# Kernel optimization log

Measured on AMD Instinct MI355X. Metric: run time of the kernel, lower is better.

The kernel has to match this reference:

```python
import jax, jax.numpy as jnp
import numpy as np

D, H, DH, DFF, K = 512, 8, 64, 2048, 31
B, T = 8, 1024


def _ln(x, g, b):
    m = x.mean(-1, keepdims=True)
    v = ((x - m) ** 2).mean(-1, keepdims=True)
    return (x - m) / jnp.sqrt(v + 1e-5) * g + b


def _silu(x):
    return x * jax.nn.sigmoid(x)


def _pe(t, d):
    i = jnp.arange(t, dtype=jnp.float32)[:, None]
    j = jnp.arange(0, d, 2, dtype=jnp.float32)
    ang = i * (1.0 / (10000.0 ** (j / d)))
    pe = jnp.zeros((t, d), jnp.float32)
    pe = pe.at[:, 0::2].set(jnp.sin(ang))
    pe = pe.at[:, 1::2].set(jnp.cos(ang))
    return pe


def setup_inputs() -> dict:
    key = jax.random.key(0)
    ks = iter(jax.random.split(key, 40))
    s = 0.02
    d = {
        'x': jax.random.normal(next(ks), (B, T, D), jnp.float32),
        # FF module 1
        'ff1_ln_g': jnp.ones((D,), jnp.float32), 'ff1_ln_b': jnp.zeros((D,), jnp.float32),
        'ff1_w1': jax.random.normal(next(ks), (D, DFF), jnp.float32) * s,
        'ff1_b1': jnp.zeros((DFF,), jnp.float32),
        'ff1_w2': jax.random.normal(next(ks), (DFF, D), jnp.float32) * s,
        'ff1_b2': jnp.zeros((D,), jnp.float32),
        # MHSA
        'mha_ln_g': jnp.ones((D,), jnp.float32), 'mha_ln_b': jnp.zeros((D,), jnp.float32),
        'wq': jax.random.normal(next(ks), (H, D, DH), jnp.float32) * s,
        'bq': jnp.zeros((H, DH), jnp.float32),
        'wk': jax.random.normal(next(ks), (H, D, DH), jnp.float32) * s,
        'bk': jnp.zeros((H, DH), jnp.float32),
        'wv': jax.random.normal(next(ks), (H, D, DH), jnp.float32) * s,
        'bv': jnp.zeros((H, DH), jnp.float32),
        'wo': jax.random.normal(next(ks), (D, D), jnp.float32) * s,
        'bo': jnp.zeros((D,), jnp.float32),
        # Conv module
        'cv_ln_g': jnp.ones((D,), jnp.float32), 'cv_ln_b': jnp.zeros((D,), jnp.float32),
        'cv_w1': jax.random.normal(next(ks), (2 * D, D), jnp.float32) * s,
        'cv_b1': jnp.zeros((2 * D,), jnp.float32),
        'cv_wd': jax.random.normal(next(ks), (D, D, K), jnp.float32) * s,
        'cv_bn_g': jnp.ones((D,), jnp.float32), 'cv_bn_b': jnp.zeros((D,), jnp.float32),
        'cv_w2': jax.random.normal(next(ks), (D, D), jnp.float32) * s,
        'cv_b2': jnp.zeros((D,), jnp.float32),
        # FF module 2
        'ff2_ln_g': jnp.ones((D,), jnp.float32), 'ff2_ln_b': jnp.zeros((D,), jnp.float32),
        'ff2_w1': jax.random.normal(next(ks), (D, DFF), jnp.float32) * s,
        'ff2_b1': jnp.zeros((DFF,), jnp.float32),
        'ff2_w2': jax.random.normal(next(ks), (DFF, D), jnp.float32) * s,
        'ff2_b2': jnp.zeros((D,), jnp.float32),
        # final layer norm
        'fin_g': jnp.ones((D,), jnp.float32), 'fin_b': jnp.zeros((D,), jnp.float32),
    }
    return d


def _block(x, p):
    def ffn(x, g, b, w1, b1, w2, b2):
        y = _silu(_ln(x, g, b) @ w1 + b1) @ w2 + b2
        return x + y  # FeedForwardModule internal residual

    # x = x + 0.5 * ff_1(x)
    x = x + 0.5 * ffn(x, p['ff1_ln_g'], p['ff1_ln_b'], p['ff1_w1'], p['ff1_b1'], p['ff1_w2'], p['ff1_b2'])

    # MHSA module (with its own internal residual), then block residual
    y = _ln(x, p['mha_ln_g'], p['mha_ln_b']) + _pe(x.shape[1], x.shape[2])
    q = jnp.einsum('btd,hde->bhte', y, p['wq']) + p['bq'][None, :, None, :]
    k = jnp.einsum('btd,hde->bhte', y, p['wk']) + p['bk'][None, :, None, :]
    v = jnp.einsum('btd,hde->bhte', y, p['wv']) + p['bv'][None, :, None, :]
    scores = jnp.einsum('bhtd,bhsd->bhts', q, k) * (1.0 / np.sqrt(DH))
    attn = jax.nn.softmax(scores, axis=-1)
    o = jnp.einsum('bhts,bhsd->bhtd', attn, v)
    # faithful to original: raw view [B,H,T,dh] -> [B,T,H*dh] (no transpose)
    o = o.reshape(x.shape[0], x.shape[1], H * DH)
    o = o @ p['wo'] + p['bo']
    x = x + (x + o)

    # Convolution module (internal residual), then block residual
    y = _ln(x, p['cv_ln_g'], p['cv_ln_b']).swapaxes(1, 2)  # [B,D,T]
    y = jnp.einsum('ed,bdt->bet', p['cv_w1'], y) + p['cv_b1'][None, :, None]
    a, g = jnp.split(y, 2, axis=1)
    y = a * jax.nn.sigmoid(g)  # GLU over channel dim
    y = jax.lax.conv_general_dilated(y, p['cv_wd'], (1,), [(K // 2, K // 2)],
                                     dimension_numbers=('NCH', 'OIH', 'NCH'))
    # BatchNorm1d in training mode: batch stats over (batch, time), biased variance
    m = y.mean((0, 2), keepdims=True)
    var = ((y - m) ** 2).mean((0, 2), keepdims=True)
    y = (y - m) / jnp.sqrt(var + 1e-5) * p['cv_bn_g'][None, :, None] + p['cv_bn_b'][None, :, None]
    y = _silu(y)
    y = jnp.einsum('ed,bdt->bet', p['cv_w2'], y) + p['cv_b2'][None, :, None]
    y = y.swapaxes(1, 2)
    x = x + (x + y)

    # x = x + 0.5 * ff_2(x)
    x = x + 0.5 * ffn(x, p['ff2_ln_g'], p['ff2_ln_b'], p['ff2_w1'], p['ff2_b1'], p['ff2_w2'], p['ff2_b2'])

    return _ln(x, p['fin_g'], p['fin_b'])


def reference(x, ff1_ln_g, ff1_ln_b, ff1_w1, ff1_b1, ff1_w2, ff1_b2,
              mha_ln_g, mha_ln_b, wq, bq, wk, bk, wv, bv, wo, bo,
              cv_ln_g, cv_ln_b, cv_w1, cv_b1, cv_wd, cv_bn_g, cv_bn_b, cv_w2, cv_b2,
              ff2_ln_g, ff2_ln_b, ff2_w1, ff2_b1, ff2_w2, ff2_b2,
              fin_g, fin_b):
    p = dict(ff1_ln_g=ff1_ln_g, ff1_ln_b=ff1_ln_b, ff1_w1=ff1_w1, ff1_b1=ff1_b1,
             ff1_w2=ff1_w2, ff1_b2=ff1_b2, mha_ln_g=mha_ln_g, mha_ln_b=mha_ln_b,
             wq=wq, bq=bq, wk=wk, bk=bk, wv=wv, bv=bv, wo=wo, bo=bo,
             cv_ln_g=cv_ln_g, cv_ln_b=cv_ln_b, cv_w1=cv_w1, cv_b1=cv_b1, cv_wd=cv_wd,
             cv_bn_g=cv_bn_g, cv_bn_b=cv_bn_b, cv_w2=cv_w2, cv_b2=cv_b2,
             ff2_ln_g=ff2_ln_g, ff2_ln_b=ff2_ln_b, ff2_w1=ff2_w1, ff2_b1=ff2_b1,
             ff2_w2=ff2_w2, ff2_b2=ff2_b2, fin_g=fin_g, fin_b=fin_b)
    return _block(x, p)
```

## Files before the change

### kernel.cpp

```cpp
#include <hip/hip_runtime.h>


typedef __attribute__((ext_vector_type(4))) float f32x4;
typedef __attribute__((ext_vector_type(8))) short short8;
typedef __attribute__((ext_vector_type(4))) short s16x4;

__device__ __forceinline__ float bfs2f(short s) {
  unsigned u = ((unsigned)(unsigned short)s) << 16;
  float f; __builtin_memcpy(&f, &u, 4); return f;
}
__device__ __forceinline__ short f2bfs(float f) {
  unsigned u; __builtin_memcpy(&u, &f, 4);
  u = (u + 0x7FFFu + ((u >> 16) & 1u)) >> 16;
  return (short)u;
}
__device__ __forceinline__ float sigmoidf_(float x) { return 1.f / (1.f + __expf(-x)); }

#define GLOADLDS(gsrc, ldst) \
  __builtin_amdgcn_global_load_lds((__attribute__((address_space(1))) void*)(gsrc), \
                                   (__attribute__((address_space(3))) void*)(ldst), 16, 0, 0)

#define VMCNT_ASM(n) asm volatile("s_waitcnt vmcnt(" #n ")" ::: "memory")
template<int N> __device__ __forceinline__ void vmcnt_wait() {
  if      constexpr (N == 0)  VMCNT_ASM(0);
  else if constexpr (N == 2)  VMCNT_ASM(2);
  else if constexpr (N == 3)  VMCNT_ASM(3);
  else if constexpr (N == 4)  VMCNT_ASM(4);
  else if constexpr (N == 6)  VMCNT_ASM(6);
  else if constexpr (N == 8)  VMCNT_ASM(8);
  else                        VMCNT_ASM(0);
}
#define MEMFENCE asm volatile("" ::: "memory")

enum { EPI_SILU = 0, EPI_BBIAS = 1, EPI_RES = 2, EPI_QKV = 3, EPI_F32 = 6 };

template<int BM, int BN, int WM, int WN, int EPI>
__global__ __launch_bounds__(256) void gemm_bt(
    const short* __restrict__ A, int lda, long zAh, long zAl,
    const short* __restrict__ BT, int ldbt, long zBh, long zBl,
    int K, int Kdec,
    void* C, int ldc, long zCh, long zCl, int zdiv,
    const float* bias, const float* bias2, const float* bias3,
    const float* resid, float alpha, float beta)
{
  constexpr int FM = BM / (WM * 16), FN = BN / (WN * 16);
  constexpr int AIT = (BM * 4) / 256, BIT = (BN * 4) / 256;
  constexpr int L = AIT + BIT;
  __shared__ short sA[3][BM * 32];
  __shared__ short sB[3][BN * 32];
  const int tid = threadIdx.x;
  const int zmask = (1 << zdiv) - 1;
  const int zhi = (int)(blockIdx.z >> zdiv);
  const int zlo = (int)(blockIdx.z & zmask);
  A  += (long)zhi * zAh + (long)zlo * zAl;
  BT += (long)zhi * zBh + (long)zlo * zBl;
  char* cbase = (char*)C + (long)zhi * zCh + (long)zlo * zCl;
  const int m0 = blockIdx.x * BM, n0 = blockIdx.y * BN;
  const int Keff = K - (zlo == zmask ? Kdec : 0);

  auto stage = [&](int buf, int k0) {
#pragma unroll
    for (int it = 0; it < AIT; ++it) {
      int idx = it * 256 + tid;
      GLOADLDS(A + (long)(m0 + (idx >> 2)) * lda + k0 + (idx & 3) * 8, &sA[buf][idx * 8]);
    }
#pragma unroll
    for (int it = 0; it < BIT; ++it) {
      int idx = it * 256 + tid;
      GLOADLDS(BT + (long)(n0 + (idx >> 2)) * ldbt + k0 + (idx & 3) * 8, &sB[buf][idx * 8]);
    }
  };

  f32x4 acc[FM][FN];
#pragma unroll
  for (int i = 0; i < FM; ++i) {
#pragma unroll
    for (int j = 0; j < FN; ++j) acc[i][j] = (f32x4){0.f, 0.f, 0.f, 0.f};
  }
  const int lane = tid & 63, wid = tid >> 6;
  const int wm = wid / WN, wn = wid % WN;
  const int lr = lane & 15, kg = lane >> 4;
  const int aRow = wm * (BM / WM), bRow = wn * (BN / WN);

  const int nt = Keff >> 5;
  stage(0, 0);
  stage(1, 32);
  vmcnt_wait<L>();
  __builtin_amdgcn_s_barrier();

  int cur = 0, sbuf = 2;
  for (int t = 0; t < nt; ++t) {
    const bool st = (t + 2 < nt);
    if (st) stage(sbuf, (t + 2) * 32);
    short8 af[FM], bfr[FN];
#pragma unroll
    for (int mi = 0; mi < FM; ++mi)
      af[mi] = *(const short8*)&sA[cur][(aRow + mi * 16 + lr) * 32 + kg * 8];
#pragma unroll
    for (int ni = 0; ni < FN; ++ni)
      bfr[ni] = *(const short8*)&sB[cur][(bRow + ni * 16 + lr) * 32 + kg * 8];
    __builtin_amdgcn_s_setprio(1);
#pragma unroll
    for (int mi = 0; mi < FM; ++mi) {
#pragma unroll
      for (int ni = 0; ni < FN; ++ni)
        acc[mi][ni] = __builtin_amdgcn_mfma_f32_16x16x32_bf16(af[mi], bfr[ni], acc[mi][ni], 0, 0, 0);
    }
    __builtin_amdgcn_s_setprio(0);
    if (st) vmcnt_wait<L>(); else vmcnt_wait<0>();
    __builtin_amdgcn_s_barrier();
    cur = (cur == 2) ? 0 : cur + 1;
    sbuf = (sbuf == 2) ? 0 : sbuf + 1;
  }

  const int baseRow = m0 + aRow, baseCol = n0 + bRow;
#pragma unroll
  for (int mi = 0; mi < FM; ++mi) {
#pragma unroll
    for (int ni = 0; ni < FN; ++ni) {
      const int col = baseCol + ni * 16 + lr;
#pragma unroll
      for (int r = 0; r < 4; ++r) {
        const int row = baseRow + mi * 16 + kg * 4 + r;
        float v = acc[mi][ni][r];
        if (EPI == EPI_SILU) {
          v += bias[col];
          v = v * sigmoidf_(v);
          ((short*)cbase)[(long)row * ldc + col] = f2bfs(v);
        } else if (EPI == EPI_BBIAS) {
          v += bias[col];
          ((short*)cbase)[(long)row * ldc + col] = f2bfs(v);
        } else if (EPI == EPI_RES) {
          v += bias[col];
          float rv = resid[(long)row * ldc + col];
          ((float*)cbase)[(long)row * ldc + col] = alpha * rv + beta * v;
        } else if (EPI == EPI_QKV) {
          if (col < 512)       v = (v + bias[col]) * 0.125f;
          else if (col < 1024) v += bias2[col - 512];
          else                 v += bias3[col - 1024];
          ((short*)cbase)[(long)row * ldc + col] = f2bfs(v);
        } else if (EPI == EPI_F32) {
          ((float*)cbase)[(long)row * ldc + col] = v;
        }
      }
    }
  }
}

__global__ __launch_bounds__(256) void conv_tap(
    const short* __restrict__ glu,
    const short* __restrict__ wdP,
    short* __restrict__ parts)
{
  __shared__ short sA[2][144 * 32];
  const int tid = threadIdx.x;
  const int bid = blockIdx.x;
  const int cc = bid & 7, j = bid >> 3;
  const int y = cc >> 1, kg = cc & 1;
  const int x = j & 7, b = j >> 3;
  const int m0 = x * 128, n0 = y * 128;
  const short* Arow0 = glu + ((long)b * 1056 + m0 + 1 + kg * 16) * 512;
  short* cbase = parts + (long)kg * (8192L * 512) + (long)b * (1024L * 512);

  const int lane = tid & 63, wid = tid >> 6;
  const int wm = wid >> 1, wn = wid & 1;
  const int lr = lane & 15, kgr = lane >> 4;
  const int aRow = wm * 64, bRow = wn * 64;

  const short* Bp = wdP + (long)((n0 + bRow) >> 4) * (512L * 512)
                  + (long)(kg * 256) * 512 + lane * 8;
  const long NSTR = 512L * 512;

  auto stageA = [&](int buf, int ib) {
#pragma unroll
    for (int it = 0; it < 3; ++it) {
      int idx = it * 256 + tid;
      if (idx < 576) {
        GLOADLDS(Arow0 + (long)(idx >> 2) * 512 + ib * 32 + (idx & 3) * 8,
                 &sA[buf][idx * 8]);
      }
    }
  };

  f32x4 acc[4][4];
#pragma unroll
  for (int i = 0; i < 4; ++i) {
#pragma unroll
    for (int jj = 0; jj < 4; ++jj) acc[i][jj] = (f32x4){0.f, 0.f, 0.f, 0.f};
  }
  short8 b0[4], b1[4];

  stageA(0, 0);
  MEMFENCE;
#pragma unroll
  for (int ni = 0; ni < 4; ++ni)
    b0[ni] = *(const short8*)(Bp + ni * NSTR);
  MEMFENCE;
  vmcnt_wait<4>();
  __builtin_amdgcn_s_barrier();

  int cur = 0;
  for (int ib = 0; ib < 16; ++ib) {
    if (ib + 1 < 16) stageA(cur ^ 1, ib + 1);
    MEMFENCE;
#pragma unroll
    for (int kk = 0; kk < 16; ++kk) {
      const long noff = (kk + 1 < 16) ? (long)((kk + 1) * 16 + ib) * 512
                                      : (long)(ib + 1) * 512;
      if ((kk & 1) == 0) {
#pragma unroll
        for (int ni = 0; ni < 4; ++ni)
          b1[ni] = *(const short8*)(Bp + noff + ni * NSTR);
      } else {
#pragma unroll
        for (int ni = 0; ni < 4; ++ni)
          b0[ni] = *(const short8*)(Bp + noff + ni * NSTR);
      }
      short8 af[4];
#pragma unroll
      for (int mi = 0; mi < 4; ++mi)
        af[mi] = *(const short8*)&sA[cur][(kk + aRow + mi * 16 + lr) * 32 + kgr * 8];
      __builtin_amdgcn_s_setprio(1);
      if ((kk & 1) == 0) {
#pragma unroll
        for (int mi = 0; mi < 4; ++mi) {
#pragma unroll
          for (int ni = 0; ni < 4; ++ni)
            acc[mi][ni] = __builtin_amdgcn_mfma_f32_16x16x32_bf16(af[mi], b0[ni], acc[mi][ni], 0, 0, 0);
        }
      } else {
#pragma unroll
        for (int mi = 0; mi < 4; ++mi) {
#pragma unroll
          for (int ni = 0; ni < 4; ++ni)
            acc[mi][ni] = __builtin_amdgcn_mfma_f32_16x16x32_bf16(af[mi], b1[ni], acc[mi][ni], 0, 0, 0);
        }
      }
      __builtin_amdgcn_s_setprio(0);
    }
    vmcnt_wait<4>();
    __builtin_amdgcn_s_barrier();
    cur ^= 1;
  }
  vmcnt_wait<0>();

  const int baseRow = m0 + aRow, baseCol = n0 + bRow;
#pragma unroll
  for (int mi = 0; mi < 4; ++mi) {
#pragma unroll
    for (int ni = 0; ni < 4; ++ni) {
      const int col = baseCol + ni * 16 + lr;
#pragma unroll
      for (int r = 0; r < 4; ++r) {
        const int row = baseRow + mi * 16 + kgr * 4 + r;
        cbase[(long)row * 512 + col] = f2bfs(acc[mi][ni][r]);
      }
    }
  }
}

__global__ __launch_bounds__(256) void flash_attn(
    const short* __restrict__ qkv,
    const short* __restrict__ vt,
    short* __restrict__ out)
{
  __shared__ short sQ[64 * 64];
  __shared__ short sK[64 * 64];
  __shared__ short sV[64 * 64];
  __shared__ short sP[4][16 * 64];
  const int tid = threadIdx.x;
  const int lane = tid & 63, w = tid >> 6;
  const int lr = lane & 15, kg = lane >> 4;
  const int bh = (int)blockIdx.z;
  const int b = bh >> 3, h = bh & 7;
  const int q0 = blockIdx.x * 64;
  const short* qbase = qkv + (long)b * 1024 * 1536 + h * 64;
  const short* kbase = qbase + 512;
  const short* vtb = vt + (long)bh * 65536;

#pragma unroll
  for (int it = 0; it < 2; ++it) {
    int idx = it * 256 + tid;
    int row = idx >> 3, c = (idx & 7) ^ (row & 7);
    GLOADLDS(qbase + (long)(q0 + row) * 1536 + c * 8, &sQ[idx * 8]);
  }
  __syncthreads();
  short8 bq[2];
#pragma unroll
  for (int ks = 0; ks < 2; ++ks)
    bq[ks] = *(const short8*)&sQ[(w * 16 + lr) * 64 + ((ks * 4 + kg) ^ (lr & 7)) * 8];

  f32x4 po[4];
#pragma unroll
  for (int mi = 0; mi < 4; ++mi) po[mi] = (f32x4){0.f, 0.f, 0.f, 0.f};
  float m = -3.0e38f, l = 0.f;

  for (int s0 = 0; s0 < 1024; s0 += 64) {
#pragma unroll
    for (int it = 0; it < 2; ++it) {
      int idx = it * 256 + tid;
      int row = idx >> 3, c = (idx & 7) ^ (row & 7);
      GLOADLDS(kbase + (long)(s0 + row) * 1536 + c * 8, &sK[idx * 8]);
    }
#pragma unroll
    for (int it = 0; it < 2; ++it) {
      int idx = it * 256 + tid;
      int row = idx >> 3, c = (idx & 7) ^ (row & 7);
      GLOADLDS(vtb + (long)row * 1024 + s0 + c * 8, &sV[idx * 8]);
    }
    __syncthreads();

    f32x4 as[4];
#pragma unroll
    for (int mi = 0; mi < 4; ++mi) as[mi] = (f32x4){0.f, 0.f, 0.f, 0.f};
    __builtin_amdgcn_s_setprio(1);
#pragma unroll
    for (int ks = 0; ks < 2; ++ks) {
#pragma unroll
      for (int mi = 0; mi < 4; ++mi) {
        short8 ak = *(const short8*)&sK[(mi * 16 + lr) * 64 + ((ks * 4 + kg) ^ (lr & 7)) * 8];
        as[mi] = __builtin_amdgcn_mfma_f32_16x16x32_bf16(ak, bq[ks], as[mi], 0, 0, 0);
      }
    }
    __builtin_amdgcn_s_setprio(0);

    float rmax = as[0][0];
#pragma unroll
    for (int mi = 0; mi < 4; ++mi) {
#pragma unroll
      for (int r = 0; r < 4; ++r) rmax = fmaxf(rmax, as[mi][r]);
    }
    rmax = fmaxf(rmax, __shfl_xor(rmax, 16));
    rmax = fmaxf(rmax, __shfl_xor(rmax, 32));
    const float mn = fmaxf(m, rmax);
    const float sc = __expf(m - mn);
    float p[4][4];
    float rsum = 0.f;
#pragma unroll
    for (int mi = 0; mi < 4; ++mi) {
#pragma unroll
      for (int r = 0; r < 4; ++r) { p[mi][r] = __expf(as[mi][r] - mn); rsum += p[mi][r]; }
    }
    rsum += __shfl_xor(rsum, 16);
    rsum += __shfl_xor(rsum, 32);
    l = l * sc + rsum;
    m = mn;
#pragma unroll
    for (int mi = 0; mi < 4; ++mi) {
#pragma unroll
      for (int r = 0; r < 4; ++r) po[mi][r] *= sc;
    }
#pragma unroll
    for (int mi = 0; mi < 4; ++mi) {
      s16x4 pk;
#pragma unroll
      for (int r = 0; r < 4; ++r) pk[r] = f2bfs(p[mi][r]);
      *(s16x4*)&sP[w][lr * 64 + ((mi ^ (lr & 3)) * 16 + kg * 4)] = pk;
    }
    __builtin_amdgcn_s_setprio(1);
#pragma unroll
    for (int ks = 0; ks < 2; ++ks) {
      short8 bp = *(const short8*)&sP[w][lr * 64 + (((ks * 2 + (kg >> 1)) ^ (lr & 3)) * 16 + (kg & 1) * 8)];
#pragma unroll
      for (int mi = 0; mi < 4; ++mi) {
        short8 av = *(const short8*)&sV[(mi * 16 + lr) * 64 + ((ks * 4 + kg) ^ (lr & 7)) * 8];
        po[mi] = __builtin_amdgcn_mfma_f32_16x16x32_bf16(av, bp, po[mi], 0, 0, 0);
      }
    }
    __builtin_amdgcn_s_setprio(0);
    __syncthreads();
  }

  const float inv = 1.f / l;
  const int t2 = q0 + w * 16 + lr;
  const int n = h * 1024 + t2;
  short* ob = out + ((long)b * 1024 + (n >> 3)) * 512 + (n & 7) * 64;
#pragma unroll
  for (int mi = 0; mi < 4; ++mi) {
    s16x4 o;
#pragma unroll
    for (int r = 0; r < 4; ++r) o[r] = f2bfs(po[mi][r] * inv);
    *(s16x4*)&ob[mi * 16 + kg * 4] = o;
  }
}

__global__ __launch_bounds__(256) void reduce_bn(
    const short* __restrict__ parts, long pstride,
    short* __restrict__ z, float* stats)
{
  const int r0 = blockIdx.x * 16;
  const int c = threadIdx.x * 2;
  float s0 = 0.f, s1 = 0.f, q0 = 0.f, q1 = 0.f;
#pragma unroll 4
  for (int r = 0; r < 16; ++r) {
    const long idx = (long)(r0 + r) * 512 + c;
    int p0 = *(const int*)&parts[idx];
    int p1 = *(const int*)&parts[idx + pstride];
    float a0 = bfs2f((short)(p0 & 0xffff)) + bfs2f((short)(p1 & 0xffff));
    float a1 = bfs2f((short)(p0 >> 16)) + bfs2f((short)(p1 >> 16));
    int zo = ((int)(unsigned short)f2bfs(a0)) | (((int)(unsigned short)f2bfs(a1)) << 16);
    *(int*)&z[idx] = zo;
    s0 += a0; s1 += a1; q0 += a0 * a0; q1 += a1 * a1;
  }
  atomicAdd(&stats[c], s0);
  atomicAdd(&stats[c + 1], s1);
  atomicAdd(&stats[512 + c], q0);
  atomicAdd(&stats[512 + c + 1], q1);
}

template<int ADDPE, int OUTF32>
__global__ __launch_bounds__(256) void ln_rows(
    const float* __restrict__ X, const float* __restrict__ g, const float* __restrict__ b,
    const float* __restrict__ pe, void* __restrict__ Y)
{
  const int row = blockIdx.x * 4 + (threadIdx.x >> 6);
  const int lane = threadIdx.x & 63;
  const int c0 = lane * 8;
  const float* src = X + (long)row * 512 + c0;
  f32x4 a = *(const f32x4*)src, c = *(const f32x4*)(src + 4);
  float x[8] = {a[0], a[1], a[2], a[3], c[0], c[1], c[2], c[3]};
  float s = 0.f, q = 0.f;
#pragma unroll
  for (int j = 0; j < 8; ++j) { s += x[j]; q += x[j] * x[j]; }
#pragma unroll
  for (int off = 32; off > 0; off >>= 1) { s += __shfl_xor(s, off); q += __shfl_xor(q, off); }
  const float mean = s * (1.f / 512.f);
  const float var = q * (1.f / 512.f) - mean * mean;
  const float rstd = rsqrtf(var + 1e-5f);
  f32x4 g0 = *(const f32x4*)(g + c0), g1 = *(const f32x4*)(g + c0 + 4);
  f32x4 b0 = *(const f32x4*)(b + c0), b1 = *(const f32x4*)(b + c0 + 4);
  float gg[8] = {g0[0], g0[1], g0[2], g0[3], g1[0], g1[1], g1[2], g1[3]};
  float bb[8] = {b0[0], b0[1], b0[2], b0[3], b1[0], b1[1], b1[2], b1[3]};
  float y[8];
#pragma unroll
  for (int j = 0; j < 8; ++j) {
    y[j] = (x[j] - mean) * rstd * gg[j] + bb[j];
    if (ADDPE) y[j] += pe[(long)(row & 1023) * 512 + c0 + j];
  }
  if (OUTF32) {
    float* dst = (float*)Y + (long)row * 512 + c0;
    *(f32x4*)dst = (f32x4){y[0], y[1], y[2], y[3]};
    *(f32x4*)(dst + 4) = (f32x4){y[4], y[5], y[6], y[7]};
  } else {
    short8 o;
#pragma unroll
    for (int j = 0; j < 8; ++j) o[j] = f2bfs(y[j]);
    *(short8*)((short*)Y + (long)row * 512 + c0) = o;
  }
}

template<int INF32>
__global__ __launch_bounds__(256) void transpose64(
    const void* __restrict__ in_, int ldin, short* __restrict__ out, int ldout,
    int ctiles, int zshift, long zh_in, long zl_in, long z_out)
{
  __shared__ short t[64][72];
  const int z = blockIdx.z;
  const long inoff = (long)(z >> zshift) * zh_in + (long)(z & ((1 << zshift) - 1)) * zl_in;
  const int tr = blockIdx.x / ctiles, tc = blockIdx.x % ctiles;
  short* dst = out + (long)z * z_out + (long)(tc * 64) * ldout + tr * 64;
  const int tid = threadIdx.x;
#pragma unroll
  for (int p = 0; p < 2; ++p) {
    int idx = p * 256 + tid;
    int r = idx >> 3, c8 = (idx & 7) * 8;
    if (INF32) {
      const float* src = (const float*)in_ + inoff + (long)(tr * 64 + r) * ldin + tc * 64 + c8;
      f32x4 v0 = *(const f32x4*)src, v1 = *(const f32x4*)(src + 4);
#pragma unroll
      for (int j = 0; j < 4; ++j) { t[r][c8 + j] = f2bfs(v0[j]); t[r][c8 + 4 + j] = f2bfs(v1[j]); }
    } else {
      const short* src = (const short*)in_ + inoff + (long)(tr * 64 + r) * ldin + tc * 64 + c8;
      short8 v = *(const short8*)src;
#pragma unroll
      for (int j = 0; j < 8; ++j) t[r][c8 + j] = v[j];
    }
  }
  __syncthreads();
#pragma unroll
  for (int p = 0; p < 2; ++p) {
    int idx = p * 256 + tid;
    int c = idx >> 3, r8 = (idx & 7) * 8;
    short8 v;
#pragma unroll
    for (int j = 0; j < 8; ++j) v[j] = t[r8 + j][c];
    *(short8*)(dst + (long)c * ldout + r8) = v;
  }
}

__global__ __launch_bounds__(256) void wd_pack(const float* __restrict__ wd, short* __restrict__ wdP)
{
  const int gid = blockIdx.x * 256 + threadIdx.x;
  const int e = gid >> 9, i = gid & 511;
  const float* src = wd + ((long)e * 512 + i) * 31;
  const long rowtile = (long)(e >> 4) * (512L * 512);
  const int inner = ((i >> 3) & 3) * 128 + (e & 15) * 8 + (i & 7);
#pragma unroll
  for (int KK = 0; KK < 31; ++KK)
    wdP[rowtile + (long)(KK * 16 + (i >> 5)) * 512 + inner] = f2bfs(src[KK]);
  wdP[rowtile + (long)(31 * 16 + (i >> 5)) * 512 + inner] = 0;
}

__global__ __launch_bounds__(256) void pe_init(float* __restrict__ pe)
{
  const int gid = blockIdx.x * 256 + threadIdx.x;
  const int t = gid >> 8, p = gid & 255;
  const float freq = __expf(-(float)p * (9.210340371976184f / 256.f));
  const float ang = (float)t * freq;
  pe[(long)t * 512 + 2 * p]     = sinf(ang);
  pe[(long)t * 512 + 2 * p + 1] = cosf(ang);
}

__global__ __launch_bounds__(256) void halo_zero(short* __restrict__ gp)
{
  const int gid = blockIdx.x * 256 + threadIdx.x;
  if (gid >= 16512) return;
  long row;
  int c8;
  if (gid < 16384) {
    const int b = gid >> 11;
    const int r = (gid >> 6) & 31;
    c8 = (gid & 63) * 8;
    row = (long)b * 1056 + ((r < 16) ? r : (1024 + r));
  } else {
    const int k = gid - 16384;
    c8 = (k & 63) * 8;
    row = 8448 + (k >> 6);
  }
  *(short8*)(gp + row * 512 + c8) = (short8){0, 0, 0, 0, 0, 0, 0, 0};
}

__global__ __launch_bounds__(256) void glu_kernel(const short* __restrict__ y1, short* __restrict__ gp)
{
  const int gid = blockIdx.x * 256 + threadIdx.x;
  const int row = gid >> 7;
  const int ci = (gid & 127) * 4;
  const short* base = y1 + (long)row * 1024;
  s16x4 a = *(const s16x4*)(base + ci);
  s16x4 g = *(const s16x4*)(base + 512 + ci);
  const int b = row >> 10, t = row & 1023;
  s16x4 o;
#pragma unroll
  for (int j = 0; j < 4; ++j) o[j] = f2bfs(bfs2f(a[j]) * sigmoidf_(bfs2f(g[j])));
  *(s16x4*)(gp + ((long)b * 1056 + 16 + t) * 512 + ci) = o;
}

__global__ void bn_stats(float* stats, const float* __restrict__ bn_g, const float* __restrict__ bn_b)
{
  const int c = blockIdx.x * 256 + threadIdx.x;
  if (c < 512) {
    float mean = stats[c] * (1.f / 8192.f);
    float var = stats[512 + c] * (1.f / 8192.f) - mean * mean;
    float sc = bn_g[c] * rsqrtf(var + 1e-5f);
    stats[1024 + c] = sc;
    stats[1536 + c] = bn_b[c] - mean * sc;
  }
}

__global__ __launch_bounds__(256) void bn_silu(const short* __restrict__ z, const float* __restrict__ stats,
                                               short* __restrict__ out)
{
  const long base = ((long)blockIdx.x * 256 + threadIdx.x) * 8;
  const int c0 = (int)(base & 511);
  short8 v = *(const short8*)(z + base);
  short8 o;
#pragma unroll
  for (int j = 0; j < 8; ++j) {
    const int c = c0 + j;
    float y = bfs2f(v[j]) * stats[1024 + c] + stats[1536 + c];
    o[j] = f2bfs(y * sigmoidf_(y));
  }
  *(short8*)(out + base) = o;
}

__global__ __launch_bounds__(256) void cast_bf16(const float* __restrict__ in, short* __restrict__ out, long n)
{
  for (long i = (long)blockIdx.x * 256 + threadIdx.x; i < n; i += (long)gridDim.x * 256)
    out[i] = f2bfs(in[i]);
}

extern "C" void kernel_launch(void* const* d_in, const int* in_sizes, int n_in,
                              void* d_out, int out_size, void* d_ws, size_t ws_size,
                              hipStream_t stream)
{
  (void)in_sizes; (void)n_in; (void)out_size; (void)ws_size;
  const float* x_in   = (const float*)d_in[0];
  const float* ff1_g  = (const float*)d_in[1];
  const float* ff1_bb = (const float*)d_in[2];
  const float* ff1_w1 = (const float*)d_in[3];
  const float* ff1_b1 = (const float*)d_in[4];
  const float* ff1_w2 = (const float*)d_in[5];
  const float* ff1_b2 = (const float*)d_in[6];
  const float* mha_g  = (const float*)d_in[7];
  const float* mha_b  = (const float*)d_in[8];
  const float* wq     = (const float*)d_in[9];
  const float* bq     = (const float*)d_in[10];
  const float* wk     = (const float*)d_in[11];
  const float* bk     = (const float*)d_in[12];
  const float* wv     = (const float*)d_in[13];
  const float* bv     = (const float*)d_in[14];
  const float* wo     = (const float*)d_in[15];
  const float* bo     = (const float*)d_in[16];
  const float* cv_g   = (const float*)d_in[17];
  const float* cv_b   = (const float*)d_in[18];
  const float* cv_w1  = (const float*)d_in[19];
  const float* cv_b1  = (const float*)d_in[20];
  const float* cv_wd  = (const float*)d_in[21];
  const float* bn_g   = (const float*)d_in[22];
  const float* bn_b   = (const float*)d_in[23];
  const float* cv_w2  = (const float*)d_in[24];
  const float* cv_b2  = (const float*)d_in[25];
  const float* ff2_g  = (const float*)d_in[26];
  const float* ff2_b  = (const float*)d_in[27];
  const float* ff2_w1 = (const float*)d_in[28];
  const float* ff2_b1 = (const float*)d_in[29];
  const float* ff2_w2 = (const float*)d_in[30];
  const float* ff2_b2 = (const float*)d_in[31];
  const float* fin_g  = (const float*)d_in[32];
  const float* fin_b  = (const float*)d_in[33];

  size_t off = 0;
  char* wsb = (char*)d_ws;
  auto take = [&](size_t n) { char* p = wsb + off; off += (n + 255) & ~(size_t)255; return p; };
  short* ff1w1T = (short*)take(2048L * 512 * 2);
  short* ff1w2T = (short*)take(512L * 2048 * 2);
  short* qkvT   = (short*)take(1536L * 512 * 2);
  short* woT    = (short*)take(512L * 512 * 2);
  short* cw1b   = (short*)take(1024L * 512 * 2);
  short* cw2b   = (short*)take(512L * 512 * 2);
  short* wdP    = (short*)take(32L * 512 * 512 * 2);
  short* ff2w1T = (short*)take(2048L * 512 * 2);
  short* ff2w2T = (short*)take(512L * 2048 * 2);
  float* xcur   = (float*)take(8192L * 512 * 4);
  char*  Ra     = take(8192L * 2048 * 2);
  short* Rb     = (short*)take(8192L * 512 * 2);
  short* Rg     = (short*)take((8L * 1056 + 2) * 512 * 2);
  short* parts  = (short*)take(2L * 8192 * 512 * 2);
  short* vt     = (short*)take(64L * 64 * 1024 * 2);
  float* pe     = (float*)take(1024L * 512 * 4);
  float* stats  = (float*)take(2048L * 4);

  short* hid = (short*)Ra;
  short* qkv = (short*)Ra;
  short* y1  = (short*)Ra;

  transpose64<1><<<dim3(256, 1, 1), 256, 0, stream>>>(ff1_w1, 2048, ff1w1T, 512, 32, 0, 0, 0, 0);
  transpose64<1><<<dim3(256, 1, 1), 256, 0, stream>>>(ff1_w2, 512, ff1w2T, 2048, 8, 0, 0, 0, 0);
  transpose64<1><<<dim3(8, 1, 8), 256, 0, stream>>>(wq, 64, qkvT, 512, 1, 0, 32768, 0, 32768);
  transpose64<1><<<dim3(8, 1, 8), 256, 0, stream>>>(wk, 64, qkvT + 512 * 512, 512, 1, 0, 32768, 0, 32768);
  transpose64<1><<<dim3(8, 1, 8), 256, 0, stream>>>(wv, 64, qkvT + 1024 * 512, 512, 1, 0, 32768, 0, 32768);
  transpose64<1><<<dim3(64, 1, 1), 256, 0, stream>>>(wo, 512, woT, 512, 8, 0, 0, 0, 0);
  transpose64<1><<<dim3(256, 1, 1), 256, 0, stream>>>(ff2_w1, 2048, ff2w1T, 512, 32, 0, 0, 0, 0);
  transpose64<1><<<dim3(256, 1, 1), 256, 0, stream>>>(ff2_w2, 512, ff2w2T, 2048, 8, 0, 0, 0, 0);
  wd_pack<<<1024, 256, 0, stream>>>(cv_wd, wdP);
  pe_init<<<1024, 256, 0, stream>>>(pe);
  cast_bf16<<<2048, 256, 0, stream>>>(cv_w1, cw1b, 524288L);
  cast_bf16<<<1024, 256, 0, stream>>>(cv_w2, cw2b, 262144L);

  ln_rows<0, 0><<<2048, 256, 0, stream>>>(x_in, ff1_g, ff1_bb, nullptr, Rb);
  gemm_bt<128, 128, 2, 2, EPI_SILU><<<dim3(64, 16, 1), 256, 0, stream>>>(
      Rb, 512, 0, 0, ff1w1T, 512, 0, 0, 512, 0,
      hid, 2048, 0, 0, 0, ff1_b1, nullptr, nullptr, nullptr, 0.f, 0.f);
  gemm_bt<64, 64, 2, 2, EPI_RES><<<dim3(128, 8, 1), 256, 0, stream>>>(
      hid, 2048, 0, 0, ff1w2T, 2048, 0, 0, 2048, 0,
      xcur, 512, 0, 0, 0, ff1_b2, nullptr, nullptr, x_in, 1.5f, 0.5f);

  ln_rows<1, 0><<<2048, 256, 0, stream>>>(xcur, mha_g, mha_b, pe, Rb);
  gemm_bt<128, 128, 2, 2, EPI_QKV><<<dim3(64, 12, 1), 256, 0, stream>>>(
      Rb, 512, 0, 0, qkvT, 512, 0, 0, 512, 0,
      qkv, 1536, 0, 0, 0, bq, bk, bv, nullptr, 0.f, 0.f);
  transpose64<0><<<dim3(16, 1, 64), 256, 0, stream>>>(qkv + 1024, 1536, vt, 1024, 1, 3,
                                                      1024L * 1536, 64, 65536);
  flash_attn<<<dim3(16, 1, 64), 256, 0, stream>>>(qkv, vt, Rb);
  gemm_bt<64, 64, 2, 2, EPI_RES><<<dim3(128, 8, 1), 256, 0, stream>>>(
      Rb, 512, 0, 0, woT, 512, 0, 0, 512, 0,
      xcur, 512, 0, 0, 0, bo, nullptr, nullptr, xcur, 2.f, 1.f);

  ln_rows<0, 0><<<2048, 256, 0, stream>>>(xcur, cv_g, cv_b, nullptr, Rb);
  gemm_bt<128, 128, 2, 2, EPI_BBIAS><<<dim3(64, 8, 1), 256, 0, stream>>>(
      Rb, 512, 0, 0, cw1b, 512, 0, 0, 512, 0,
      y1, 1024, 0, 0, 0, cv_b1, nullptr, nullptr, nullptr, 0.f, 0.f);
  halo_zero<<<65, 256, 0, stream>>>(Rg);
  glu_kernel<<<4096, 256, 0, stream>>>(y1, Rg);
  (void)hipMemsetAsync(stats, 0, 1024 * sizeof(float), stream);
  conv_tap<<<512, 256, 0, stream>>>(Rg, wdP, parts);
  reduce_bn<<<512, 256, 0, stream>>>(parts, 8192L * 512, Rb, stats);
  bn_stats<<<2, 256, 0, stream>>>(stats, bn_g, bn_b);
  bn_silu<<<2048, 256, 0, stream>>>(Rb, stats, (short*)Rg);
  gemm_bt<64, 64, 2, 2, EPI_RES><<<dim3(128, 8, 1), 256, 0, stream>>>(
      (short*)Rg, 512, 0, 0, cw2b, 512, 0, 0, 512, 0,
      xcur, 512, 0, 0, 0, cv_b2, nullptr, nullptr, xcur, 2.f, 1.f);

  ln_rows<0, 0><<<2048, 256, 0, stream>>>(xcur, ff2_g, ff2_b, nullptr, Rb);
  gemm_bt<128, 128, 2, 2, EPI_SILU><<<dim3(64, 16, 1), 256, 0, stream>>>(
      Rb, 512, 0, 0, ff2w1T, 512, 0, 0, 512, 0,
      hid, 2048, 0, 0, 0, ff2_b1, nullptr, nullptr, nullptr, 0.f, 0.f);
  gemm_bt<64, 64, 2, 2, EPI_RES><<<dim3(128, 8, 1), 256, 0, stream>>>(
      hid, 2048, 0, 0, ff2w2T, 2048, 0, 0, 2048, 0,
      xcur, 512, 0, 0, 0, ff2_b2, nullptr, nullptr, xcur, 1.5f, 0.5f);

  ln_rows<0, 1><<<2048, 256, 0, stream>>>(xcur, fin_g, fin_b, nullptr, (float*)d_out);
}
```

Before: 498.2 us.

## Add direct-B GEMM with pre-packed MFMA-fragment weights for N=512 residual GEMMs

Adds a packB kernel that lays out weight matrices in MFMA-fragment order, so each lane can load its B fragment straight from global memory into registers. A new gemm_bd kernel (64x128 tiles, triple-buffered LDS for A only, double-buffered B registers) replaces the 64x64 gemm_bt used by the four residual-epilogue GEMMs (ff1 w2, wo, conv w2, ff2 w2). The goal is to cut LDS traffic and B staging, and to raise tile size over the previous configuration. The cost is more global B reads per block, since B is not shared through LDS, and hand-tuned vmcnt accounting that has to stay correct.

```diff
diff --git a/kernel.cpp b/kernel.cpp
--- a/kernel.cpp
+++ b/kernel.cpp
@@ -26,6 +26,7 @@
   else if constexpr (N == 2)  VMCNT_ASM(2);
   else if constexpr (N == 3)  VMCNT_ASM(3);
   else if constexpr (N == 4)  VMCNT_ASM(4);
+  else if constexpr (N == 5)  VMCNT_ASM(5);
   else if constexpr (N == 6)  VMCNT_ASM(6);
   else if constexpr (N == 8)  VMCNT_ASM(8);
   else                        VMCNT_ASM(0);
@@ -145,6 +146,130 @@
       }
     }
   }
+}
+
+template<int NT>
+__global__ __launch_bounds__(256) void gemm_bd(
+    const short* __restrict__ A,
+    const short* __restrict__ wBP,
+    const float* __restrict__ bias,
+    const float* __restrict__ resid,
+    float* __restrict__ C,
+    float alpha, float beta)
+{
+  constexpr int K = NT * 32;
+  __shared__ short sA[3][64 * 32];
+  const int tid = threadIdx.x;
+  const int x = (int)blockIdx.x >> 2, y = (int)blockIdx.x & 3;
+  const int m0 = x * 64, n0 = y * 128;
+  const int lane = tid & 63, wid = tid >> 6;
+  const int wm = wid >> 1, wn = wid & 1;
+  const int lr = lane & 15, kgr = lane >> 4;
+  const int aRow = wm * 32, bRow = wn * 64;
+  const long NSTR = (long)NT * 512;
+  const short* Bp = wBP + (long)((n0 + bRow) >> 4) * NSTR + lane * 8;
+
+  auto stageA = [&](int buf, int t) {
+    GLOADLDS(A + (long)(m0 + (tid >> 2)) * K + t * 32 + (tid & 3) * 8, &sA[buf][tid * 8]);
+  };
+
+  f32x4 acc[2][4];
+#pragma unroll
+  for (int i = 0; i < 2; ++i) {
+#pragma unroll
+    for (int j = 0; j < 4; ++j) acc[i][j] = (f32x4){0.f, 0.f, 0.f, 0.f};
+  }
+  short8 b0[4], b1[4];
+
+  stageA(0, 0);
+  stageA(1, 1);
+  MEMFENCE;
+#pragma unroll
+  for (int ni = 0; ni < 4; ++ni)
+    b0[ni] = *(const short8*)(Bp + ni * NSTR);
+  MEMFENCE;
+  vmcnt_wait<5>();
+  __builtin_amdgcn_s_barrier();
+
+  int rd = 0;
+  for (int t = 0; t < NT; t += 2) {
+    {
+      int wr = rd - 1; if (wr < 0) wr += 3;
+      if (t + 2 < NT) stageA(wr, t + 2);
+      MEMFENCE;
+#pragma unroll
+      for (int ni = 0; ni < 4; ++ni)
+        b1[ni] = *(const short8*)(Bp + (long)(t + 1) * 512 + ni * NSTR);
+      MEMFENCE;
+      short8 af[2];
+#pragma unroll
+      for (int mi = 0; mi < 2; ++mi)
+        af[mi] = *(const short8*)&sA[rd][(aRow + mi * 16 + lr) * 32 + kgr * 8];
+      __builtin_amdgcn_s_setprio(1);
+#pragma unroll
+      for (int mi = 0; mi < 2; ++mi) {
+#pragma unroll
+        for (int ni = 0; ni < 4; ++ni)
+          acc[mi][ni] = __builtin_amdgcn_mfma_f32_16x16x32_bf16(af[mi], b0[ni], acc[mi][ni], 0, 0, 0);
+      }
+      __builtin_amdgcn_s_setprio(0);
+      if (t + 2 < NT) vmcnt_wait<5>(); else vmcnt_wait<4>();
+      __builtin_amdgcn_s_barrier();
+      rd = (rd == 2) ? 0 : rd + 1;
+    }
+    {
+      int wr = rd - 1; if (wr < 0) wr += 3;
+      if (t + 3 < NT) stageA(wr, t + 3);
+      MEMFENCE;
+      if (t + 2 < NT) {
+#pragma unroll
+        for (int ni = 0; ni < 4; ++ni)
+          b0[ni] = *(const short8*)(Bp + (long)(t + 2) * 512 + ni * NSTR);
+      }
+      MEMFENCE;
+      short8 af[2];
+#pragma unroll
+      for (int mi = 0; mi < 2; ++mi)
+        af[mi] = *(const short8*)&sA[rd][(aRow + mi * 16 + lr) * 32 + kgr * 8];
+      __builtin_amdgcn_s_setprio(1);
+#pragma unroll
+      for (int mi = 0; mi < 2; ++mi) {
+#pragma unroll
+        for (int ni = 0; ni < 4; ++ni)
+          acc[mi][ni] = __builtin_amdgcn_mfma_f32_16x16x32_bf16(af[mi], b1[ni], acc[mi][ni], 0, 0, 0);
+      }
+      __builtin_amdgcn_s_setprio(0);
+      if (t + 3 < NT) vmcnt_wait<5>(); else vmcnt_wait<0>();
+      __builtin_amdgcn_s_barrier();
+      rd = (rd == 2) ? 0 : rd + 1;
+    }
+  }
+
+  const int baseRow = m0 + aRow, baseCol = n0 + bRow;
+#pragma unroll
+  for (int mi = 0; mi < 2; ++mi) {
+#pragma unroll
+    for (int ni = 0; ni < 4; ++ni) {
+      const int col = baseCol + ni * 16 + lr;
+#pragma unroll
+      for (int r = 0; r < 4; ++r) {
+        const int row = baseRow + mi * 16 + kgr * 4 + r;
+        float v = acc[mi][ni][r] + bias[col];
+        float rv = resid[(long)row * 512 + col];
+        C[(long)row * 512 + col] = alpha * rv + beta * v;
+      }
+    }
+  }
+}
+
+template<int TRANS, int KSHIFT>
+__global__ __launch_bounds__(256) void packB(const float* __restrict__ in, short* __restrict__ out)
+{
+  const int gid = blockIdx.x * 256 + threadIdx.x;
+  const int n = gid >> KSHIFT;
+  const int k = gid & ((1 << KSHIFT) - 1);
+  const float v = TRANS ? in[(long)k * 512 + n] : in[((long)n << KSHIFT) | k];
+  out[((long)((n >> 4) << (KSHIFT - 5)) + (k >> 5)) * 512 + ((k >> 3) & 3) * 128 + (n & 15) * 8 + (k & 7)] = f2bfs(v);
 }
 
 __global__ __launch_bounds__(256) void conv_tap(
@@ -623,14 +748,14 @@
   char* wsb = (char*)d_ws;
   auto take = [&](size_t n) { char* p = wsb + off; off += (n + 255) & ~(size_t)255; return p; };
   short* ff1w1T = (short*)take(2048L * 512 * 2);
-  short* ff1w2T = (short*)take(512L * 2048 * 2);
+  short* ff1w2P = (short*)take(2048L * 512 * 2);
   short* qkvT   = (short*)take(1536L * 512 * 2);
-  short* woT    = (short*)take(512L * 512 * 2);
+  short* woP    = (short*)take(512L * 512 * 2);
   short* cw1b   = (short*)take(1024L * 512 * 2);
-  short* cw2b   = (short*)take(512L * 512 * 2);
+  short* cw2P   = (short*)take(512L * 512 * 2);
   short* wdP    = (short*)take(32L * 512 * 512 * 2);
   short* ff2w1T = (short*)take(2048L * 512 * 2);
-  short* ff2w2T = (short*)take(512L * 2048 * 2);
+  short* ff2w2P = (short*)take(2048L * 512 * 2);
   float* xcur   = (float*)take(8192L * 512 * 4);
   char*  Ra     = take(8192L * 2048 * 2);
   short* Rb     = (short*)take(8192L * 512 * 2);
@@ -645,25 +770,23 @@
   short* y1  = (short*)Ra;
 
   transpose64<1><<<dim3(256, 1, 1), 256, 0, stream>>>(ff1_w1, 2048, ff1w1T, 512, 32, 0, 0, 0, 0);
-  transpose64<1><<<dim3(256, 1, 1), 256, 0, stream>>>(ff1_w2, 512, ff1w2T, 2048, 8, 0, 0, 0, 0);
+  packB<1, 11><<<4096, 256, 0, stream>>>(ff1_w2, ff1w2P);
   transpose64<1><<<dim3(8, 1, 8), 256, 0, stream>>>(wq, 64, qkvT, 512, 1, 0, 32768, 0, 32768);
   transpose64<1><<<dim3(8, 1, 8), 256, 0, stream>>>(wk, 64, qkvT + 512 * 512, 512, 1, 0, 32768, 0, 32768);
   transpose64<1><<<dim3(8, 1, 8), 256, 0, stream>>>(wv, 64, qkvT + 1024 * 512, 512, 1, 0, 32768, 0, 32768);
-  transpose64<1><<<dim3(64, 1, 1), 256, 0, stream>>>(wo, 512, woT, 512, 8, 0, 0, 0, 0);
+  packB<1, 9><<<1024, 256, 0, stream>>>(wo, woP);
   transpose64<1><<<dim3(256, 1, 1), 256, 0, stream>>>(ff2_w1, 2048, ff2w1T, 512, 32, 0, 0, 0, 0);
-  transpose64<1><<<dim3(256, 1, 1), 256, 0, stream>>>(ff2_w2, 512, ff2w2T, 2048, 8, 0, 0, 0, 0);
+  packB<1, 11><<<4096, 256, 0, stream>>>(ff2_w2, ff2w2P);
+  packB<0, 9><<<1024, 256, 0, stream>>>(cv_w2, cw2P);
   wd_pack<<<1024, 256, 0, stream>>>(cv_wd, wdP);
   pe_init<<<1024, 256, 0, stream>>>(pe);
   cast_bf16<<<2048, 256, 0, stream>>>(cv_w1, cw1b, 524288L);
-  cast_bf16<<<1024, 256, 0, stream>>>(cv_w2, cw2b, 262144L);
 
   ln_rows<0, 0><<<2048, 256, 0, stream>>>(x_in, ff1_g, ff1_bb, nullptr, Rb);
   gemm_bt<128, 128, 2, 2, EPI_SILU><<<dim3(64, 16, 1), 256, 0, stream>>>(
       Rb, 512, 0, 0, ff1w1T, 512, 0, 0, 512, 0,
       hid, 2048, 0, 0, 0, ff1_b1, nullptr, nullptr, nullptr, 0.f, 0.f);
-  gemm_bt<64, 64, 2, 2, EPI_RES><<<dim3(128, 8, 1), 256, 0, stream>>>(
-      hid, 2048, 0, 0, ff1w2T, 2048, 0, 0, 2048, 0,
-      xcur, 512, 0, 0, 0, ff1_b2, nullptr, nullptr, x_in, 1.5f, 0.5f);
+  gemm_bd<64><<<512, 256, 0, stream>>>(hid, ff1w2P, ff1_b2, x_in, xcur, 1.5f, 0.5f);
 
   ln_rows<1, 0><<<2048, 256, 0, stream>>>(xcur, mha_g, mha_b, pe, Rb);
   gemm_bt<128, 128, 2, 2, EPI_QKV><<<dim3(64, 12, 1), 256, 0, stream>>>(
@@ -672,9 +795,7 @@
   transpose64<0><<<dim3(16, 1, 64), 256, 0, stream>>>(qkv + 1024, 1536, vt, 1024, 1, 3,
                                                       1024L * 1536, 64, 65536);
   flash_attn<<<dim3(16, 1, 64), 256, 0, stream>>>(qkv, vt, Rb);
-  gemm_bt<64, 64, 2, 2, EPI_RES><<<dim3(128, 8, 1), 256, 0, stream>>>(
-      Rb, 512, 0, 0, woT, 512, 0, 0, 512, 0,
-      xcur, 512, 0, 0, 0, bo, nullptr, nullptr, xcur, 2.f, 1.f);
+  gemm_bd<16><<<512, 256, 0, stream>>>(Rb, woP, bo, xcur, xcur, 2.f, 1.f);
 
   ln_rows<0, 0><<<2048, 256, 0, stream>>>(xcur, cv_g, cv_b, nullptr, Rb);
   gemm_bt<128, 128, 2, 2, EPI_BBIAS><<<dim3(64, 8, 1), 256, 0, stream>>>(
@@ -687,17 +808,13 @@
   reduce_bn<<<512, 256, 0, stream>>>(parts, 8192L * 512, Rb, stats);
   bn_stats<<<2, 256, 0, stream>>>(stats, bn_g, bn_b);
   bn_silu<<<2048, 256, 0, stream>>>(Rb, stats, (short*)Rg);
-  gemm_bt<64, 64, 2, 2, EPI_RES><<<dim3(128, 8, 1), 256, 0, stream>>>(
-      (short*)Rg, 512, 0, 0, cw2b, 512, 0, 0, 512, 0,
-      xcur, 512, 0, 0, 0, cv_b2, nullptr, nullptr, xcur, 2.f, 1.f);
+  gemm_bd<16><<<512, 256, 0, stream>>>((short*)Rg, cw2P, cv_b2, xcur, xcur, 2.f, 1.f);
 
   ln_rows<0, 0><<<2048, 256, 0, stream>>>(xcur, ff2_g, ff2_b, nullptr, Rb);
   gemm_bt<128, 128, 2, 2, EPI_SILU><<<dim3(64, 16, 1), 256, 0, stream>>>(
       Rb, 512, 0, 0, ff2w1T, 512, 0, 0, 512, 0,
       hid, 2048, 0, 0, 0, ff2_b1, nullptr, nullptr, nullptr, 0.f, 0.f);
-  gemm_bt<64, 64, 2, 2, EPI_RES><<<dim3(128, 8, 1), 256, 0, stream>>>(
-      hid, 2048, 0, 0, ff2w2T, 2048, 0, 0, 2048, 0,
-      xcur, 512, 0, 0, 0, ff2_b2, nullptr, nullptr, xcur, 1.5f, 0.5f);
+  gemm_bd<64><<<512, 256, 0, stream>>>(hid, ff2w2P, ff2_b2, xcur, xcur, 1.5f, 0.5f);
 
   ln_rows<0, 1><<<2048, 256, 0, stream>>>(xcur, fin_g, fin_b, nullptr, (float*)d_out);
 }
```

Measured after the change: 491.9 us. About the same (-1.3%).
